# Kernel optimization log

Measured on AMD Instinct MI355X. Metric: run time of the kernel, lower is better.

## Reference

```python
import jax, jax.numpy as jnp
import numpy as np

NUM_HEADS = 8
D_MODEL = 512
HEAD_DIM = D_MODEL // NUM_HEADS


def _conv1x1(x, W, b):
    # Conv1d(kernel_size=1): x [B, Cin, N], W [Cout, Cin], b [Cout] -> [B, Cout, N]
    return jnp.einsum('oi,bin->bon', W, x) + b[None, :, None]


def setup_inputs() -> dict:
    key = jax.random.key(0)
    ks = jax.random.split(key, 12)
    B, D, N, Mlen = 4, D_MODEL, 2048, 2048
    inp = {
        'query': jax.random.normal(ks[0], (B, D, N), dtype=jnp.float32),
        'key':   jax.random.normal(ks[1], (B, D, Mlen), dtype=jnp.float32),
        'value': jax.random.normal(ks[2], (B, D, Mlen), dtype=jnp.float32),
        'M':     jnp.ones((B, N, Mlen), dtype=jnp.int32),
    }
    scale = 0.02
    inp['Wq'] = jax.random.normal(ks[3], (D, D), dtype=jnp.float32) * scale
    inp['bq'] = jnp.zeros((D,), dtype=jnp.float32)
    inp['Wk'] = jax.random.normal(ks[4], (D, D), dtype=jnp.float32) * scale
    inp['bk'] = jnp.zeros((D,), dtype=jnp.float32)
    inp['Wv'] = jax.random.normal(ks[5], (D, D), dtype=jnp.float32) * scale
    inp['bv'] = jnp.zeros((D,), dtype=jnp.float32)
    inp['Wm'] = jax.random.normal(ks[6], (D, D), dtype=jnp.float32) * scale
    inp['bm'] = jnp.zeros((D,), dtype=jnp.float32)
    return inp


def reference(query, key, value, M, Wq, bq, Wk, bk, Wv, bv, Wm, bm):
    B = query.shape[0]
    # 1x1-conv projections, then channel split as [head_dim, heads] (matches torch .view)
    q = _conv1x1(query, Wq, bq).reshape(B, HEAD_DIM, NUM_HEADS, -1)  # [B, d, h, N]
    k = _conv1x1(key,   Wk, bk).reshape(B, HEAD_DIM, NUM_HEADS, -1)  # [B, d, h, M]
    v = _conv1x1(value, Wv, bv).reshape(B, HEAD_DIM, NUM_HEADS, -1)  # [B, d, h, M]
    scores = jnp.einsum('bdhn,bdhm->bhnm', q, k) / jnp.sqrt(jnp.float32(HEAD_DIM))
    # mask: positions with M==0 are disallowed -> fill with -finfo.max
    bad = (1 - M)[:, None, :, :].astype(bool)  # [B, 1, N, M], broadcasts over heads
    scores = jnp.where(bad, -jnp.finfo(scores.dtype).max, scores)
    prob = jax.nn.softmax(scores, axis=-1)  # [B, h, N, M]
    x = jnp.einsum('bhnm,bdhm->bdhn', prob, v)  # [B, d, h, N]
    out = _conv1x1(x.reshape(B, HEAD_DIM * NUM_HEADS, -1), Wm, bm)  # [B, D, N]
    return out
```

## Files before the change

### kernel.cpp

```cpp
#include <hip/hip_runtime.h>

typedef __attribute__((ext_vector_type(8))) short s8v;
typedef __attribute__((ext_vector_type(4))) float f4v;
typedef _Float16 h8 __attribute__((ext_vector_type(8)));
typedef unsigned short u16;
typedef unsigned long long u64;

#define DM 512
#define NH 8
#define HD 64
#define BB 4
#define NN 2048

extern "C" __device__ float __ocml_native_exp2_f32(float);
__device__ __forceinline__ float fexp2(float x){ return __ocml_native_exp2_f32(x); }

__device__ __forceinline__ float bf2f(u16 x){ return __uint_as_float(((unsigned)x)<<16); }
__device__ __forceinline__ u16 f2bf(float f){
  unsigned u = __float_as_uint(f);
  u += 0x7FFFu + ((u>>16)&1u);
  return (u16)(u>>16);
}
__device__ __forceinline__ void gl2lds16(const u16* g, u16* l){
  __builtin_amdgcn_global_load_lds((__attribute__((address_space(1))) void*)(g),
                                   (__attribute__((address_space(3))) void*)(l), 16, 0, 0);
}

__global__ __launch_bounds__(256) void k_maskpack(const int* M, u64* bits){
  int tid = threadIdx.x;
  int wv = tid>>6, lane = tid&63;
  size_t w0 = (size_t)blockIdx.x*64 + wv*16;
  #pragma unroll
  for (int it=0; it<16; it++){
    int v = M[(w0+it)*64 + lane];
    u64 bal = __ballot(v == 1);
    if (lane == 0) bits[w0+it] = bal;
  }
}

__global__ void k_prep(const float* Wq, const float* bq, const float* Wk, const float* bk,
                       const float* Wv, const float* bv, const float* Wm,
                       u16* Wp, u16* Wmp, float* bp,
                       const u64* bits, u64* allw){
  int blk = blockIdx.x, tid = threadIdx.x;
  if (blk < 1536){
    int t = blk >> 9, op = blk & 511;
    int srow = ((op & 63) << 3) | (op >> 6);
    const float* W = (t==0) ? Wq : ((t==1) ? Wk : Wv);
    for (int j = tid; j < 512; j += 256)
      Wp[((size_t)t*512 + op)*512 + j] = f2bf(W[(size_t)srow*512 + j]);
  } else if (blk < 2048){
    int o = blk - 1536;
    for (int c = tid; c < 512; c += 256){
      int scol = ((c & 63) << 3) | (c >> 6);
      Wmp[(size_t)o*512 + c] = f2bf(Wm[(size_t)o*512 + scol]);
    }
  } else if (blk == 2048){
    for (int idx = tid; idx < 1536; idx += 256){
      int t = idx >> 9, op = idx & 511;
      const float* bs = (t==0) ? bq : ((t==1) ? bk : bv);
      int srow = ((op & 63) << 3) | (op >> 6);
      bp[idx] = bs[srow];
    }
  } else {
    __shared__ u64 red[256];
    int bnt = blk - 2049;
    int mt = tid & 31, rg = tid >> 5;
    const u64* base = bits + (size_t)bnt*64*32;
    u64 v = ~0ull;
    #pragma unroll
    for (int j=0;j<8;j++) v &= base[(size_t)(rg*8+j)*32 + mt];
    red[tid] = v;
    __syncthreads();
    if (tid < 32){
      u64 a = red[tid];
      #pragma unroll
      for (int g2=1; g2<8; g2++) a &= red[g2*32 + tid];
      allw[(size_t)bnt*32 + tid] = a;
    }
  }
}

__global__ __launch_bounds__(256) void k_transpose(const float* q, const float* k, const float* v, u16* XT){
  __shared__ u16 T[64*72];
  int blk = blockIdx.x, tid = threadIdx.x;
  int rt = blk & 31; blk >>= 5;
  int it = blk & 7;  blk >>= 3;
  int b  = blk & 3;  int t = blk >> 2;
  const float* src = (t==0) ? q : ((t==1) ? k : v);
  src += (size_t)b*DM*NN;
  int i0 = it*64, r0 = rt*64;
  int il = tid>>4, rj = (tid&15)*4;
  #pragma unroll
  for (int p=0;p<4;p++){
    int i = il + p*16;
    float4 vv = *(const float4*)&src[(size_t)(i0+i)*NN + r0 + rj];
    float fv[4] = {vv.x, vv.y, vv.z, vv.w};
    #pragma unroll
    for (int qq=0;qq<4;qq++){
      int r = rj + qq;
      int sr = ((r&3)<<4) | (r>>2);
      T[sr*72 + i] = f2bf(fv[qq]);
    }
  }
  __syncthreads();
  u16* dst = XT + ((size_t)(t*4+b)*NN)*DM;
  int rl = tid>>3, ib = (tid&7)*8;
  #pragma unroll
  for (int p=0;p<2;p++){
    int r = rl + p*32;
    int sr = ((r&3)<<4) | (r>>2);
    s8v vv = *(s8v*)&T[sr*72 + ib];
    *(s8v*)&dst[(size_t)(r0+r)*DM + i0 + ib] = vv;
  }
}

__global__ __launch_bounds__(256) void k_proj(const u16* XT, const u16* Wp, const float* bp,
                                              u16* P, u16* VT){
  __shared__ u16 Al[128*32];
  __shared__ u16 Bl[128*32];
  __shared__ u16 S[128*72];
  int blk = blockIdx.x, tid = threadIdx.x;
  int nt = blk / 192; int mt = blk % 192;
  int tb = mt >> 4;
  int t  = tb >> 2, b = tb & 3;
  int r0 = (mt & 15)*128, o0 = nt*128;
  const u16* Abase = XT + ((size_t)tb*NN + r0)*DM;
  const u16* Bbase = Wp + ((size_t)t*512 + o0)*DM;

  int w = tid>>6, L = tid&63, li = L&15, lq = L>>4;
  int wr = w>>1, wc = w&1;
  int srow = tid>>2;
  int g8   = ((tid&3) ^ ((tid>>3)&3))*8;
  u16* AldsW = &Al[((tid&192))*8];
  u16* BldsW = &Bl[((tid&192))*8];
  int sw = (li>>1)&3;

  f4v acc[4][4];
  #pragma unroll
  for (int a=0;a<4;a++)
    #pragma unroll
    for (int c2=0;c2<4;c2++) acc[a][c2] = (f4v){0.f,0.f,0.f,0.f};

  for (int kk=0; kk<16; kk++){
    int k0 = kk*32;
    __syncthreads();
    #pragma unroll
    for (int c=0;c<2;c++){
      gl2lds16(&Abase[(size_t)(srow + c*64)*DM + k0 + g8], AldsW + c*2048);
      gl2lds16(&Bbase[(size_t)(srow + c*64)*DM + k0 + g8], BldsW + c*2048);
    }
    __syncthreads();
    s8v af[4], bfr[4];
    #pragma unroll
    for (int a=0;a<4;a++){
      int r = wr*64 + a*16 + li;
      af[a] = *(s8v*)&Al[r*32 + ((lq ^ sw))*8];
    }
    #pragma unroll
    for (int c2=0;c2<4;c2++){
      int r = wc*64 + c2*16 + li;
      bfr[c2] = *(s8v*)&Bl[r*32 + ((lq ^ sw))*8];
    }
    #pragma unroll
    for (int a=0;a<4;a++)
      #pragma unroll
      for (int c2=0;c2<4;c2++)
        acc[a][c2] = __builtin_amdgcn_mfma_f32_16x16x32_bf16(af[a], bfr[c2], acc[a][c2], 0, 0, 0);
  }

  if (t < 2){
    float scale = (t==0) ? 0.18033688f : 1.0f;
    #pragma unroll
    for (int p=0;p<2;p++){
      if (wc == p){
        #pragma unroll
        for (int c2=0;c2<4;c2++){
          int cl = c2*16 + li;
          float bias = bp[t*512 + o0 + p*64 + cl];
          #pragma unroll
          for (int a=0;a<4;a++)
            #pragma unroll
            for (int ri=0;ri<4;ri++)
              S[(wr*64 + a*16 + lq*4 + ri)*72 + cl] = f2bf((acc[a][c2][ri] + bias)*scale);
        }
      }
      __syncthreads();
      int row = tid>>1, cb = (tid&1)*32;
      int hh = (o0>>6) + p;
      u16* Pb = P + (((size_t)tb*NH + hh)*NN + r0 + row)*HD + cb;
      #pragma unroll
      for (int c=0;c<4;c++){
        s8v vv = *(s8v*)&S[row*72 + cb + c*8];
        *(s8v*)&Pb[c*8] = vv;
      }
      __syncthreads();
    }
  } else {
    int mp = mt & 15;
    #pragma unroll
    for (int p=0;p<2;p++){
      if (wc == p){
        #pragma unroll
        for (int c2=0;c2<4;c2++){
          int cl = c2*16 + li;
          float bias = bp[2*512 + o0 + p*64 + cl];
          #pragma unroll
          for (int a=0;a<4;a++)
            #pragma unroll
            for (int ri=0;ri<4;ri++){
              _Float16 hh = (_Float16)(acc[a][c2][ri] + bias);
              S[(wr*64 + a*16 + lq*4 + ri)*72 + cl] = *(const u16*)&hh;
            }
        }
      }
      __syncthreads();
      int hh = (o0>>6) + p;
      u16* Vbw = VT + ((size_t)(b*NH + hh)*16 + mp)*8192;
      #pragma unroll
      for (int it2=0; it2<4; it2++){
        int c = tid + it2*256;
        int w2  = c >> 8;
        int d   = (c >> 2) & 63;
        int lq2 = c & 3;
        u16 tmp[8];
        #pragma unroll
        for (int t2=0;t2<8;t2++){
          int ml = ((t2>>2)<<6) + w2*16 + lq2*4 + (t2&3);
          tmp[t2] = S[ml*72 + d];
        }
        *(s8v*)&Vbw[(size_t)w2*2048 + d*32 + lq2*8] = *(s8v*)&tmp[0];
      }
      __syncthreads();
    }
  }
}

__global__ __launch_bounds__(256) void k_flash(const u16* Pq, const u16* VT, const u64* bits,
                                               const u64* allw, u16* Xout){
  __shared__ __align__(16) char smem[18432 + 1024];
  float* Red = (float*)smem;
  float* lsb = (float*)(smem + 18432);

  int blk = blockIdx.x, tid = threadIdx.x;
  int bh = blk & 31; int nt = blk >> 5;
  int b = bh >> 3;
  int n0 = nt*64;
  const size_t TSZ = (size_t)BB*NH*NN*HD;
  const u16* Qb = Pq + ((size_t)bh*NN + n0)*HD;
  const u16* Kb = Pq + TSZ + (size_t)bh*NN*HD;
  const u16* Vb = VT + (size_t)bh*NN*HD;
  const u64* awp = allw + ((size_t)b*32 + nt)*32;

  int w = tid>>6, L = tid&63, li = L&15, lq = L>>4;

  s8v Qf[4][2];
  #pragma unroll
  for (int j=0;j<4;j++)
    #pragma unroll
    for (int h2=0;h2<2;h2++)
      Qf[j][h2] = *(const s8v*)&Qb[(size_t)(j*16+li)*HD + h2*32 + lq*8];

  f4v O[4][4];
  #pragma unroll
  for (int j2=0;j2<4;j2++)
    #pragma unroll
    for (int j=0;j<4;j++) O[j2][j] = (f4v){0.f,0.f,0.f,0.f};
  f4v Ols[4];
  #pragma unroll
  for (int j=0;j<4;j++) Ols[j] = (f4v){0.f,0.f,0.f,0.f};
  h8 onesV;
  #pragma unroll
  for (int e=0;e<8;e++) onesV[e] = (_Float16)1.0f;

  const u16* Krow = Kb + (size_t)(w*16 + li)*HD + lq*8;
  const u16* Vrow = Vb + (size_t)w*2048 + li*32 + lq*8;

  s8v cKA0 = *(const s8v*)&Krow[0];
  s8v cKA1 = *(const s8v*)&Krow[32];
  s8v cKB0 = *(const s8v*)&Krow[4096];
  s8v cKB1 = *(const s8v*)&Krow[4128];

  int mbit = w*16 + lq*4;

  for (int mp=0; mp<16; mp++){
    size_t noff = (size_t)((mp+1)&15)*8192;
    s8v nKA0 = *(const s8v*)&Krow[noff];
    s8v nKA1 = *(const s8v*)&Krow[noff + 32];
    s8v nKB0 = *(const s8v*)&Krow[noff + 4096];
    s8v nKB1 = *(const s8v*)&Krow[noff + 4128];
    size_t voff = (size_t)mp*8192;
    h8 cV[4];
    #pragma unroll
    for (int j2=0;j2<4;j2++) cV[j2] = *(const h8*)&Vrow[voff + j2*512];

    u64 awA = awp[2*mp], awB = awp[2*mp+1];
    h8 Pf[4];
    f4v S[4];

    __builtin_amdgcn_s_setprio(1);
    #pragma unroll
    for (int j=0;j<4;j++){
      f4v c = (f4v){0.f,0.f,0.f,0.f};
      c = __builtin_amdgcn_mfma_f32_16x16x32_bf16(cKA0, Qf[j][0], c, 0, 0, 0);
      c = __builtin_amdgcn_mfma_f32_16x16x32_bf16(cKA1, Qf[j][1], c, 0, 0, 0);
      S[j] = c;
    }
    __builtin_amdgcn_s_setprio(0);
    if (awA == ~0ull){
      #pragma unroll
      for (int j=0;j<4;j++){
        Pf[j][0] = (_Float16)fexp2(S[j][0]);
        Pf[j][1] = (_Float16)fexp2(S[j][1]);
        Pf[j][2] = (_Float16)fexp2(S[j][2]);
        Pf[j][3] = (_Float16)fexp2(S[j][3]);
      }
    } else {
      #pragma unroll
      for (int j=0;j<4;j++){
        u64 mw = bits[((size_t)b*NN + n0 + j*16 + li)*32 + 2*mp];
        #pragma unroll
        for (int r=0;r<4;r++){
          float ev = fexp2(S[j][r]);
          Pf[j][r] = (_Float16)(((mw>>(mbit+r)) & 1ull) ? ev : 0.f);
        }
      }
    }

    __builtin_amdgcn_s_setprio(1);
    #pragma unroll
    for (int j=0;j<4;j++){
      f4v c = (f4v){0.f,0.f,0.f,0.f};
      c = __builtin_amdgcn_mfma_f32_16x16x32_bf16(cKB0, Qf[j][0], c, 0, 0, 0);
      c = __builtin_amdgcn_mfma_f32_16x16x32_bf16(cKB1, Qf[j][1], c, 0, 0, 0);
      S[j] = c;
    }
    __builtin_amdgcn_s_setprio(0);
    if (awB == ~0ull){
      #pragma unroll
      for (int j=0;j<4;j++){
        Pf[j][4] = (_Float16)fexp2(S[j][0]);
        Pf[j][5] = (_Float16)fexp2(S[j][1]);
        Pf[j][6] = (_Float16)fexp2(S[j][2]);
        Pf[j][7] = (_Float16)fexp2(S[j][3]);
      }
    } else {
      #pragma unroll
      for (int j=0;j<4;j++){
        u64 mw = bits[((size_t)b*NN + n0 + j*16 + li)*32 + 2*mp + 1];
        #pragma unroll
        for (int r=0;r<4;r++){
          float ev = fexp2(S[j][r]);
          Pf[j][4+r] = (_Float16)(((mw>>(mbit+r)) & 1ull) ? ev : 0.f);
        }
      }
    }

    __builtin_amdgcn_s_setprio(1);
    #pragma unroll
    for (int j2=0;j2<4;j2++)
      #pragma unroll
      for (int j=0;j<4;j++)
        O[j2][j] = __builtin_amdgcn_mfma_f32_16x16x32_f16(cV[j2], Pf[j], O[j2][j], 0, 0, 0);
    #pragma unroll
    for (int j=0;j<4;j++)
      Ols[j] = __builtin_amdgcn_mfma_f32_16x16x32_f16(onesV, Pf[j], Ols[j], 0, 0, 0);
    __builtin_amdgcn_s_setprio(0);

    cKA0 = nKA0; cKA1 = nKA1; cKB0 = nKB0; cKB1 = nKB1;
  }

  if (lq == 0){
    #pragma unroll
    for (int j=0;j<4;j++) lsb[w*64 + j*16 + li] = Ols[j][0];
  }
  __syncthreads();

  #pragma unroll
  for (int ph=0; ph<4; ph++){
    if (w == ph){
      #pragma unroll
      for (int j=0;j<4;j++)
        #pragma unroll
        for (int j2=0;j2<4;j2++){
          f4v* p = (f4v*)&Red[(j*16+li)*68 + j2*16 + lq*4];
          if (ph == 0) *p = O[j2][j];
          else { f4v t = *p; t += O[j2][j]; *p = t; }
        }
    }
    __syncthreads();
  }

  int n = tid>>2, d0 = (tid&3)*16;
  float s = lsb[n] + lsb[64+n] + lsb[128+n] + lsb[192+n];
  float inv = (s > 0.f) ? 1.0f/s : 0.f;
  int h = bh & 7;
  u16* Xo = Xout + ((size_t)b*NN + n0 + n)*DM + h*HD + d0;
  u16 tmp[16];
  #pragma unroll
  for (int e2=0;e2<4;e2++){
    f4v vv = *(f4v*)&Red[n*68 + d0 + e2*4];
    #pragma unroll
    for (int q2=0;q2<4;q2++) tmp[e2*4+q2] = f2bf(vv[q2]*inv);
  }
  *(s8v*)&Xo[0] = *(s8v*)&tmp[0];
  *(s8v*)&Xo[8] = *(s8v*)&tmp[8];
}

__global__ __launch_bounds__(256) void k_out(const u16* Wmp, const u16* Xout, const float* bm, float* out){
  __shared__ u16 Al[64*32];
  __shared__ u16 Bl[128*32];
  int blk = blockIdx.x, tid = threadIdx.x;
  int nt = blk & 15; blk >>= 4;
  int ot = blk & 7;  int b = blk >> 3;
  int o0 = ot*64, n0 = nt*128;
  const u16* Abase = Wmp + (size_t)o0*DM;
  const u16* Bbase = Xout + ((size_t)b*NN + n0)*DM;

  int w = tid>>6, L = tid&63, li = L&15, lq = L>>4;
  int wo = w&1, wn = w>>1;
  int srow = tid>>2;
  int g8   = ((tid&3) ^ ((tid>>3)&3))*8;
  u16* AldsW = &Al[((tid&192))*8];
  u16* BldsW = &Bl[((tid&192))*8];
  int sw = (li>>1)&3;

  f4v acc[2][4];
  #pragma unroll
  for (int a=0;a<2;a++)
    #pragma unroll
    for (int c2=0;c2<4;c2++) acc[a][c2] = (f4v){0.f,0.f,0.f,0.f};

  for (int kk=0; kk<16; kk++){
    int k0 = kk*32;
    __syncthreads();
    gl2lds16(&Abase[(size_t)srow*DM + k0 + g8], AldsW);
    #pragma unroll
    for (int c=0;c<2;c++)
      gl2lds16(&Bbase[(size_t)(srow + c*64)*DM + k0 + g8], BldsW + c*2048);
    __syncthreads();
    s8v af[2], bfr[4];
    #pragma unroll
    for (int a=0;a<2;a++){
      int r = wo*32 + a*16 + li;
      af[a] = *(s8v*)&Al[r*32 + ((lq ^ sw))*8];
    }
    #pragma unroll
    for (int c2=0;c2<4;c2++){
      int r = wn*64 + c2*16 + li;
      bfr[c2] = *(s8v*)&Bl[r*32 + ((lq ^ sw))*8];
    }
    #pragma unroll
    for (int a=0;a<2;a++)
      #pragma unroll
      for (int c2=0;c2<4;c2++)
        acc[a][c2] = __builtin_amdgcn_mfma_f32_16x16x32_bf16(af[a], bfr[c2], acc[a][c2], 0, 0, 0);
  }

  #pragma unroll
  for (int a=0;a<2;a++){
    #pragma unroll
    for (int ri=0;ri<4;ri++){
      int o = o0 + wo*32 + a*16 + lq*4 + ri;
      float bias = bm[o];
      float* ob = out + ((size_t)b*DM + o)*NN + n0 + wn*64;
      #pragma unroll
      for (int c2=0;c2<4;c2++)
        ob[c2*16 + li] = acc[a][c2][ri] + bias;
    }
  }
}

extern "C" void kernel_launch(void* const* d_in, const int* in_sizes, int n_in,
                              void* d_out, int out_size, void* d_ws, size_t ws_size,
                              hipStream_t stream){
  const float* q  = (const float*)d_in[0];
  const float* k  = (const float*)d_in[1];
  const float* v  = (const float*)d_in[2];
  const int*   M  = (const int*)d_in[3];
  const float* Wq = (const float*)d_in[4];
  const float* bq = (const float*)d_in[5];
  const float* Wk = (const float*)d_in[6];
  const float* bk = (const float*)d_in[7];
  const float* Wv = (const float*)d_in[8];
  const float* bv = (const float*)d_in[9];
  const float* Wm = (const float*)d_in[10];
  const float* bm = (const float*)d_in[11];

  char* ws = (char*)d_ws;
  u16*   XT   = (u16*)(ws + 0);
  u16*   P    = (u16*)(ws + 25165824);
  u16*   VT   = (u16*)(ws + 41943040);
  u16*   Wp   = (u16*)(ws + 50331648);
  u16*   Wmp  = (u16*)(ws + 51904512);
  float* bp   = (float*)(ws + 52428800);
  u64*   bits = (u64*)(ws + 52434944);
  u16*   Xout = (u16*)(ws + 54532096);
  u64*   allw = (u64*)(ws + 62920704);
  float* out  = (float*)d_out;

  k_maskpack<<<4096, 256, 0, stream>>>(M, bits);
  k_prep<<<2177, 256, 0, stream>>>(Wq, bq, Wk, bk, Wv, bv, Wm, Wp, Wmp, bp, bits, allw);
  k_transpose<<<3072, 256, 0, stream>>>(q, k, v, XT);
  k_proj<<<768, 256, 0, stream>>>(XT, Wp, bp, P, VT);
  k_flash<<<1024, 256, 0, stream>>>(P, VT, bits, allw, Xout);
  k_out<<<512, 256, 0, stream>>>(Wmp, Xout, bm, out);
}
```

Baseline: 280.2 us.

## Split flash waves 2x2 over key and query tiles to halve cross-wave reduction

Changes the flash-attention wave decomposition from four waves each owning a 16-key slice for all 64 queries to a 2x2 grid. Each wave now handles 32 keys for 32 queries, which halves the per-wave O accumulators and cuts the cross-wave reduction from four phases to two. It also drops the software prefetch of next-iteration K, loading K and V in the current iteration instead, and adds a launch-bounds occupancy hint of 3 blocks. Each wave now loads twice the K/V data per iteration, and the loss of prefetching may expose more load latency.

```diff
diff --git a/kernel.cpp b/kernel.cpp
--- a/kernel.cpp
+++ b/kernel.cpp
@@ -236,8 +236,8 @@
   }
 }
 
-__global__ __launch_bounds__(256) void k_flash(const u16* Pq, const u16* VT, const u64* bits,
-                                               const u64* allw, u16* Xout){
+__global__ __launch_bounds__(256, 3) void k_flash(const u16* Pq, const u16* VT, const u64* bits,
+                                                  const u64* allw, u16* Xout){
   __shared__ __align__(16) char smem[18432 + 1024];
   float* Red = (float*)smem;
   float* lsb = (float*)(smem + 18432);
@@ -253,105 +253,125 @@
   const u64* awp = allw + ((size_t)b*32 + nt)*32;
 
   int w = tid>>6, L = tid&63, li = L&15, lq = L>>4;
-
-  s8v Qf[4][2];
-  #pragma unroll
-  for (int j=0;j<4;j++)
+  int wm = w>>1, wn = w&1;
+
+  s8v Qf[2][2];
+  #pragma unroll
+  for (int jj=0;jj<2;jj++)
     #pragma unroll
     for (int h2=0;h2<2;h2++)
-      Qf[j][h2] = *(const s8v*)&Qb[(size_t)(j*16+li)*HD + h2*32 + lq*8];
-
-  f4v O[4][4];
+      Qf[jj][h2] = *(const s8v*)&Qb[(size_t)((wn*2+jj)*16+li)*HD + h2*32 + lq*8];
+
+  f4v O[4][2];
   #pragma unroll
   for (int j2=0;j2<4;j2++)
     #pragma unroll
-    for (int j=0;j<4;j++) O[j2][j] = (f4v){0.f,0.f,0.f,0.f};
-  f4v Ols[4];
-  #pragma unroll
-  for (int j=0;j<4;j++) Ols[j] = (f4v){0.f,0.f,0.f,0.f};
+    for (int jj=0;jj<2;jj++) O[j2][jj] = (f4v){0.f,0.f,0.f,0.f};
+  f4v Ols[2];
+  #pragma unroll
+  for (int jj=0;jj<2;jj++) Ols[jj] = (f4v){0.f,0.f,0.f,0.f};
   h8 onesV;
   #pragma unroll
   for (int e=0;e<8;e++) onesV[e] = (_Float16)1.0f;
 
-  const u16* Krow = Kb + (size_t)(w*16 + li)*HD + lq*8;
-  const u16* Vrow = Vb + (size_t)w*2048 + li*32 + lq*8;
-
-  s8v cKA0 = *(const s8v*)&Krow[0];
-  s8v cKA1 = *(const s8v*)&Krow[32];
-  s8v cKB0 = *(const s8v*)&Krow[4096];
-  s8v cKB1 = *(const s8v*)&Krow[4128];
-
-  int mbit = w*16 + lq*4;
+  const u16* Krow0 = Kb + (size_t)((wm*2+0)*16 + li)*HD + lq*8;
+  const u16* Krow1 = Kb + (size_t)((wm*2+1)*16 + li)*HD + lq*8;
+  const u16* Vrow0 = Vb + (size_t)(wm*2+0)*2048 + li*32 + lq*8;
+  const u16* Vrow1 = Vb + (size_t)(wm*2+1)*2048 + li*32 + lq*8;
+  const u64* bitsL = bits + ((size_t)b*NN + n0)*32;
+
+  int mbit0 = (wm*2+0)*16 + lq*4;
+  int mbit1 = (wm*2+1)*16 + lq*4;
 
   for (int mp=0; mp<16; mp++){
-    size_t noff = (size_t)((mp+1)&15)*8192;
-    s8v nKA0 = *(const s8v*)&Krow[noff];
-    s8v nKA1 = *(const s8v*)&Krow[noff + 32];
-    s8v nKB0 = *(const s8v*)&Krow[noff + 4096];
-    s8v nKB1 = *(const s8v*)&Krow[noff + 4128];
-    size_t voff = (size_t)mp*8192;
-    h8 cV[4];
-    #pragma unroll
-    for (int j2=0;j2<4;j2++) cV[j2] = *(const h8*)&Vrow[voff + j2*512];
+    size_t off = (size_t)mp*8192;
+    s8v kA0_0 = *(const s8v*)&Krow0[off];
+    s8v kA1_0 = *(const s8v*)&Krow0[off + 32];
+    s8v kA0_1 = *(const s8v*)&Krow1[off];
+    s8v kA1_1 = *(const s8v*)&Krow1[off + 32];
+    s8v kB0_0 = *(const s8v*)&Krow0[off + 4096];
+    s8v kB1_0 = *(const s8v*)&Krow0[off + 4128];
+    s8v kB0_1 = *(const s8v*)&Krow1[off + 4096];
+    s8v kB1_1 = *(const s8v*)&Krow1[off + 4128];
 
     u64 awA = awp[2*mp], awB = awp[2*mp+1];
-    h8 Pf[4];
-    f4v S[4];
-
+    h8 Pf0[2], Pf1[2];
+
+    f4v SA0[2], SA1[2];
     __builtin_amdgcn_s_setprio(1);
     #pragma unroll
-    for (int j=0;j<4;j++){
+    for (int jj=0;jj<2;jj++){
       f4v c = (f4v){0.f,0.f,0.f,0.f};
-      c = __builtin_amdgcn_mfma_f32_16x16x32_bf16(cKA0, Qf[j][0], c, 0, 0, 0);
-      c = __builtin_amdgcn_mfma_f32_16x16x32_bf16(cKA1, Qf[j][1], c, 0, 0, 0);
-      S[j] = c;
+      c = __builtin_amdgcn_mfma_f32_16x16x32_bf16(kA0_0, Qf[jj][0], c, 0, 0, 0);
+      c = __builtin_amdgcn_mfma_f32_16x16x32_bf16(kA1_0, Qf[jj][1], c, 0, 0, 0);
+      SA0[jj] = c;
+      f4v d = (f4v){0.f,0.f,0.f,0.f};
+      d = __builtin_amdgcn_mfma_f32_16x16x32_bf16(kA0_1, Qf[jj][0], d, 0, 0, 0);
+      d = __builtin_amdgcn_mfma_f32_16x16x32_bf16(kA1_1, Qf[jj][1], d, 0, 0, 0);
+      SA1[jj] = d;
     }
     __builtin_amdgcn_s_setprio(0);
     if (awA == ~0ull){
       #pragma unroll
-      for (int j=0;j<4;j++){
-        Pf[j][0] = (_Float16)fexp2(S[j][0]);
-        Pf[j][1] = (_Float16)fexp2(S[j][1]);
-        Pf[j][2] = (_Float16)fexp2(S[j][2]);
-        Pf[j][3] = (_Float16)fexp2(S[j][3]);
-      }
+      for (int jj=0;jj<2;jj++)
+        #pragma unroll
+        for (int r=0;r<4;r++){
+          Pf0[jj][r] = (_Float16)fexp2(SA0[jj][r]);
+          Pf1[jj][r] = (_Float16)fexp2(SA1[jj][r]);
+        }
     } else {
       #pragma unroll
-      for (int j=0;j<4;j++){
-        u64 mw = bits[((size_t)b*NN + n0 + j*16 + li)*32 + 2*mp];
+      for (int jj=0;jj<2;jj++){
+        u64 mw = bitsL[(size_t)((wn*2+jj)*16+li)*32 + 2*mp];
         #pragma unroll
         for (int r=0;r<4;r++){
-          float ev = fexp2(S[j][r]);
-          Pf[j][r] = (_Float16)(((mw>>(mbit+r)) & 1ull) ? ev : 0.f);
-        }
-      }
-    }
-
+          float e0 = fexp2(SA0[jj][r]);
+          float e1 = fexp2(SA1[jj][r]);
+          Pf0[jj][r] = (_Float16)(((mw>>(mbit0+r)) & 1ull) ? e0 : 0.f);
+          Pf1[jj][r] = (_Float16)(((mw>>(mbit1+r)) & 1ull) ? e1 : 0.f);
+        }
+      }
+    }
+
+    h8 cV0[4], cV1[4];
+    #pragma unroll
+    for (int j2=0;j2<4;j2++){
+      cV0[j2] = *(const h8*)&Vrow0[off + j2*512];
+      cV1[j2] = *(const h8*)&Vrow1[off + j2*512];
+    }
+
+    f4v SB0[2], SB1[2];
     __builtin_amdgcn_s_setprio(1);
     #pragma unroll
-    for (int j=0;j<4;j++){
+    for (int jj=0;jj<2;jj++){
       f4v c = (f4v){0.f,0.f,0.f,0.f};
-      c = __builtin_amdgcn_mfma_f32_16x16x32_bf16(cKB0, Qf[j][0], c, 0, 0, 0);
-      c = __builtin_amdgcn_mfma_f32_16x16x32_bf16(cKB1, Qf[j][1], c, 0, 0, 0);
-      S[j] = c;
+      c = __builtin_amdgcn_mfma_f32_16x16x32_bf16(kB0_0, Qf[jj][0], c, 0, 0, 0);
+      c = __builtin_amdgcn_mfma_f32_16x16x32_bf16(kB1_0, Qf[jj][1], c, 0, 0, 0);
+      SB0[jj] = c;
+      f4v d = (f4v){0.f,0.f,0.f,0.f};
+      d = __builtin_amdgcn_mfma_f32_16x16x32_bf16(kB0_1, Qf[jj][0], d, 0, 0, 0);
+      d = __builtin_amdgcn_mfma_f32_16x16x32_bf16(kB1_1, Qf[jj][1], d, 0, 0, 0);
+      SB1[jj] = d;
     }
     __builtin_amdgcn_s_setprio(0);
     if (awB == ~0ull){
       #pragma unroll
-      for (int j=0;j<4;j++){
-        Pf[j][4] = (_Float16)fexp2(S[j][0]);
-        Pf[j][5] = (_Float16)fexp2(S[j][1]);
-        Pf[j][6] = (_Float16)fexp2(S[j][2]);
-        Pf[j][7] = (_Float16)fexp2(S[j][3]);
-      }
+      for (int jj=0;jj<2;jj++)
+        #pragma unroll
+        for (int r=0;r<4;r++){
+          Pf0[jj][4+r] = (_Float16)fexp2(SB0[jj][r]);
+          Pf1[jj][4+r] = (_Float16)fexp2(SB1[jj][r]);
+        }
     } else {
       #pragma unroll
-      for (int j=0;j<4;j++){
-        u64 mw = bits[((size_t)b*NN + n0 + j*16 + li)*32 + 2*mp + 1];
+      for (int jj=0;jj<2;jj++){
+        u64 mw = bitsL[(size_t)((wn*2+jj)*16+li)*32 + 2*mp + 1];
         #pragma unroll
         for (int r=0;r<4;r++){
-          float ev = fexp2(S[j][r]);
-          Pf[j][4+r] = (_Float16)(((mw>>(mbit+r)) & 1ull) ? ev : 0.f);
+          float e0 = fexp2(SB0[jj][r]);
+          float e1 = fexp2(SB1[jj][r]);
+          Pf0[jj][4+r] = (_Float16)(((mw>>(mbit0+r)) & 1ull) ? e0 : 0.f);
+          Pf1[jj][4+r] = (_Float16)(((mw>>(mbit1+r)) & 1ull) ? e1 : 0.f);
         }
       }
     }
@@ -360,39 +380,41 @@
     #pragma unroll
     for (int j2=0;j2<4;j2++)
       #pragma unroll
-      for (int j=0;j<4;j++)
-        O[j2][j] = __builtin_amdgcn_mfma_f32_16x16x32_f16(cV[j2], Pf[j], O[j2][j], 0, 0, 0);
-    #pragma unroll
-    for (int j=0;j<4;j++)
-      Ols[j] = __builtin_amdgcn_mfma_f32_16x16x32_f16(onesV, Pf[j], Ols[j], 0, 0, 0);
+      for (int jj=0;jj<2;jj++){
+        O[j2][jj] = __builtin_amdgcn_mfma_f32_16x16x32_f16(cV0[j2], Pf0[jj], O[j2][jj], 0, 0, 0);
+        O[j2][jj] = __builtin_amdgcn_mfma_f32_16x16x32_f16(cV1[j2], Pf1[jj], O[j2][jj], 0, 0, 0);
+      }
+    #pragma unroll
+    for (int jj=0;jj<2;jj++){
+      Ols[jj] = __builtin_amdgcn_mfma_f32_16x16x32_f16(onesV, Pf0[jj], Ols[jj], 0, 0, 0);
+      Ols[jj] = __builtin_amdgcn_mfma_f32_16x16x32_f16(onesV, Pf1[jj], Ols[jj], 0, 0, 0);
+    }
     __builtin_amdgcn_s_setprio(0);
-
-    cKA0 = nKA0; cKA1 = nKA1; cKB0 = nKB0; cKB1 = nKB1;
   }
 
   if (lq == 0){
     #pragma unroll
-    for (int j=0;j<4;j++) lsb[w*64 + j*16 + li] = Ols[j][0];
-  }
-  __syncthreads();
-
-  #pragma unroll
-  for (int ph=0; ph<4; ph++){
-    if (w == ph){
-      #pragma unroll
-      for (int j=0;j<4;j++)
+    for (int jj=0;jj<2;jj++)
+      lsb[wm*64 + (wn*2+jj)*16 + li] = Ols[jj][0];
+  }
+
+  #pragma unroll
+  for (int ph=0; ph<2; ph++){
+    if (wm == ph){
+      #pragma unroll
+      for (int jj=0;jj<2;jj++)
         #pragma unroll
         for (int j2=0;j2<4;j2++){
-          f4v* p = (f4v*)&Red[(j*16+li)*68 + j2*16 + lq*4];
-          if (ph == 0) *p = O[j2][j];
-          else { f4v t = *p; t += O[j2][j]; *p = t; }
+          f4v* p = (f4v*)&Red[((wn*2+jj)*16+li)*68 + j2*16 + lq*4];
+          if (ph == 0) *p = O[j2][jj];
+          else { f4v t = *p; t += O[j2][jj]; *p = t; }
         }
     }
     __syncthreads();
   }
 
   int n = tid>>2, d0 = (tid&3)*16;
-  float s = lsb[n] + lsb[64+n] + lsb[128+n] + lsb[192+n];
+  float s = lsb[n] + lsb[64+n];
   float inv = (s > 0.f) ? 1.0f/s : 0.f;
   int h = bh & 7;
   u16* Xo = Xout + ((size_t)b*NN + n0 + n)*DM + h*HD + d0;
```

New measurement: 311.5 us. 11.2% more time.
